# Optimization experiments

Hardware: AMD Instinct MI355X
Metric: run time of the kernel (lower is better)

## Reference

```python
import jax, jax.numpy as jnp
import numpy as np

H = 512  # hidden size
E = 512  # embedding / input size
V = 10000  # vocab size


def _lstm_cell(x, h, c, W_ih, W_hh, b_ih, b_hh):
    # torch LSTMCell gate order: i, f, g, o
    gates = x @ W_ih.T + h @ W_hh.T + b_ih + b_hh
    i, f, g, o = jnp.split(gates, 4, axis=-1)
    i = jax.nn.sigmoid(i)
    f = jax.nn.sigmoid(f)
    g = jnp.tanh(g)
    o = jax.nn.sigmoid(o)
    c_new = f * c + i * g
    h_new = o * jnp.tanh(c_new)
    return h_new, c_new


def setup_inputs() -> dict:
    key = jax.random.key(0)
    ks = jax.random.split(key, 14)
    T, B, U = 128, 32, 1024
    s = 0.05
    return {
        "inputs": jax.random.normal(ks[0], (T, B, E), jnp.float32),
        "h0": jax.random.normal(ks[1], (2, B, H), jnp.float32),
        "c0": jax.random.normal(ks[2], (2, B, H), jnp.float32),
        "listener_outputs": jax.random.normal(ks[3], (U, B, H), jnp.float32),
        "W_ih1": jax.random.normal(ks[4], (4 * H, E), jnp.float32) * s,
        "W_hh1": jax.random.normal(ks[5], (4 * H, H), jnp.float32) * s,
        "b_ih1": jax.random.normal(ks[6], (4 * H,), jnp.float32) * s,
        "b_hh1": jax.random.normal(ks[7], (4 * H,), jnp.float32) * s,
        "W_ih2": jax.random.normal(ks[8], (4 * H, H), jnp.float32) * s,
        "W_hh2": jax.random.normal(ks[9], (4 * H, H), jnp.float32) * s,
        "b_ih2": jax.random.normal(ks[10], (4 * H,), jnp.float32) * s,
        "b_hh2": jax.random.normal(ks[11], (4 * H,), jnp.float32) * s,
        "W_out": jax.random.normal(ks[12], (V, H), jnp.float32) * s,
        "b_out": jax.random.normal(ks[13], (V,), jnp.float32) * s,
    }


def reference(inputs, h0, c0, listener_outputs,
              W_ih1, W_hh1, b_ih1, b_hh1,
              W_ih2, W_hh2, b_ih2, b_hh2,
              W_out, b_out):
    # layer-1 LSTMCell + dot-product attention per timestep
    def step1(carry, x_t):
        h1, c1 = carry
        h1, c1 = _lstm_cell(x_t, h1, c1, W_ih1, W_hh1, b_ih1, b_hh1)
        # scores over listener time U: (B, U)
        scores = jnp.einsum('ubh,bh->bu', listener_outputs, h1)
        w = jax.nn.softmax(scores, axis=1)
        ctx = jnp.einsum('ubh,bu->bh', listener_outputs, w)  # (B, H)
        return (h1, c1), ctx

    (_, _), contexts = jax.lax.scan(step1, (h0[0], c0[0]), inputs)  # (T, B, H)

    # layer-2 single-layer LSTM over attention contexts
    def step2(carry, x_t):
        h2, c2 = carry
        h2, c2 = _lstm_cell(x_t, h2, c2, W_ih2, W_hh2, b_ih2, b_hh2)
        return (h2, c2), h2

    (_, _), hs = jax.lax.scan(step2, (h0[1], c0[1]), contexts)  # (T, B, H)

    logits = hs @ W_out.T + b_out  # (T, B, V)
    return jax.nn.softmax(logits, axis=2)
```

## Files before the change

kernel.cpp:

```cpp
#include <hip/hip_runtime.h>

#define T_STEPS 128
#define BATCH   32
#define HID     512
#define EMB     512
#define ULEN    1024
#define VOCAB   10000
#define G4H     2048

#define ARR_STRIDE 16
#define GO_OFF     4096
#define GO_STRIDE  64
#define BAR_WORDS  6144

static inline int cdiv(int a, int b) { return (a + b - 1) / b; }

template <bool TRANSB>
__global__ __launch_bounds__(256)
void gemm_f32(const float* __restrict__ A, long lda, long sA,
              const float* __restrict__ Bm, long ldb, long sB,
              float* __restrict__ C, long ldc, long sC,
              int M, int N, int K, const float* __restrict__ bias)
{
    __shared__ float As[16][68];
    __shared__ float Bs[16][68];
    const int bz = blockIdx.z;
    A  += (size_t)bz * sA;
    Bm += (size_t)bz * sB;
    C  += (size_t)bz * sC;
    const int m0 = blockIdx.y * 64;
    const int n0 = blockIdx.x * 64;
    const int tid = threadIdx.x;
    const int tx = tid & 15, ty = tid >> 4;
    const int lr = tid >> 2;
    const int lk = (tid & 3) * 4;

    float acc[4][4] = {{0.f}};

    for (int k0 = 0; k0 < K; k0 += 16) {
        float4 av = *(const float4*)(A + (size_t)(m0 + lr) * lda + (k0 + lk));
        As[lk + 0][lr] = av.x; As[lk + 1][lr] = av.y;
        As[lk + 2][lr] = av.z; As[lk + 3][lr] = av.w;
        if (TRANSB) {
            const int nr = n0 + lr;
            float4 bv = make_float4(0.f, 0.f, 0.f, 0.f);
            if (nr < N) bv = *(const float4*)(Bm + (size_t)nr * ldb + (k0 + lk));
            Bs[lk + 0][lr] = bv.x; Bs[lk + 1][lr] = bv.y;
            Bs[lk + 2][lr] = bv.z; Bs[lk + 3][lr] = bv.w;
        } else {
            const int kr = tid >> 4;
            const int nc = (tid & 15) * 4;
            float4 bv = make_float4(0.f, 0.f, 0.f, 0.f);
            if (n0 + nc < N) bv = *(const float4*)(Bm + (size_t)(k0 + kr) * ldb + (n0 + nc));
            *(float4*)&Bs[kr][nc] = bv;
        }
        __syncthreads();
#pragma unroll
        for (int kk = 0; kk < 16; ++kk) {
            float ar[4], br[4];
#pragma unroll
            for (int i = 0; i < 4; i++) ar[i] = As[kk][ty * 4 + i];
#pragma unroll
            for (int j = 0; j < 4; j++) br[j] = Bs[kk][tx * 4 + j];
#pragma unroll
            for (int i = 0; i < 4; i++)
#pragma unroll
                for (int j = 0; j < 4; j++)
                    acc[i][j] += ar[i] * br[j];
        }
        __syncthreads();
    }
#pragma unroll
    for (int i = 0; i < 4; i++) {
        const int row = m0 + ty * 4 + i;
#pragma unroll
        for (int j = 0; j < 4; j++) {
            const int col = n0 + tx * 4 + j;
            if (col < N) {
                float v = acc[i][j];
                if (bias) v += bias[col];
                C[(size_t)row * ldc + col] = v;
            }
        }
    }
}

__device__ inline float sigmoidf_(float x) { return 1.f / (1.f + expf(-x)); }

__global__ __launch_bounds__(256, 1)
void lstm_scan(const float* __restrict__ gp,
               const float* __restrict__ Whh,
               const float* __restrict__ h0,
               const float* __restrict__ c0,
               float* __restrict__ h_all,
               unsigned* __restrict__ bar)
{
    __shared__ float h_lds[BATCH * HID];
    __shared__ float part[256 * 36];
    unsigned* arrive = bar;
    unsigned* go     = bar + GO_OFF;

    const int tid  = threadIdx.x;
    const int bid  = blockIdx.x;
    const int hbase = bid * 2;

    const int ks = tid >> 3;
    const int nc = tid & 7;
    const int kl = ks & 7;

    const int b    = tid >> 3;
    const int nl   = tid & 7;
    const int j    = nl & 1;
    const int lane = tid & 63;
    const int sbase = lane & ~7;
    const int n = ((nl >> 1) << 9) + hbase + j;

    float4 w0, w1, w2, w3;
    {
        const int nd = ((nc >> 1) << 9) + hbase + (nc & 1);
        const float4* wsrc = (const float4*)(Whh + (size_t)nd * HID + ks * 16);
        w0 = wsrc[0]; w1 = wsrc[1]; w2 = wsrc[2]; w3 = wsrc[3];
    }

    const float* hp0 = h_lds + ((((ks * 4 + 0) ^ kl)) << 2);
    const float* hp1 = h_lds + ((((ks * 4 + 1) ^ kl)) << 2);
    const float* hp2 = h_lds + ((((ks * 4 + 2) ^ kl)) << 2);
    const float* hp3 = h_lds + ((((ks * 4 + 3) ^ kl)) << 2);

    float c_state = (nl < 2) ? c0[b * HID + hbase + j] : 0.f;

    for (int t = 0; t < T_STEPS; ++t) {
        float gval = gp[((size_t)t * BATCH + b) * G4H + n];

        const float* hsrc = (t == 0) ? h0 : (h_all + (size_t)(t - 1) * (BATCH * HID));
#pragma unroll
        for (int i = 0; i < 16; ++i) {
            const int vi = i * 256 + tid;
            float4 v = *(const float4*)(hsrc + (size_t)vi * 4);
            const int bb = vi >> 7;
            const int f  = vi & 127;
            const int p  = f ^ ((f >> 2) & 7);
            *(float4*)&h_lds[(bb << 9) + (p << 2)] = v;
        }
        __syncthreads();

        float acc[32];
#pragma unroll
        for (int b2 = 0; b2 < 32; ++b2) {
            const int o = b2 << 9;
            float4 ha = *(const float4*)(hp0 + o);
            float4 hb = *(const float4*)(hp1 + o);
            float4 hc = *(const float4*)(hp2 + o);
            float4 hd = *(const float4*)(hp3 + o);
            acc[b2] = (ha.x * w0.x + ha.y * w0.y + ha.z * w0.z + ha.w * w0.w)
                    + (hb.x * w1.x + hb.y * w1.y + hb.z * w1.z + hb.w * w1.w)
                    + (hc.x * w2.x + hc.y * w2.y + hc.z * w2.z + hc.w * w2.w)
                    + (hd.x * w3.x + hd.y * w3.y + hd.z * w3.z + hd.w * w3.w);
        }
        {
            float* pw = &part[tid * 36];
#pragma unroll
            for (int i = 0; i < 8; ++i)
                *(float4*)(pw + i * 4) =
                    make_float4(acc[4 * i], acc[4 * i + 1], acc[4 * i + 2], acc[4 * i + 3]);
        }
        __syncthreads();

        float s = gval;
        {
            const float* pr = &part[nl * 36 + b];
#pragma unroll
            for (int kr = 0; kr < 32; ++kr) s += pr[kr * 288];
        }

        float fva = __shfl(s, sbase + 2 + j);
        float gva = __shfl(s, sbase + 4 + j);
        float ova = __shfl(s, sbase + 6 + j);
        if (nl < 2) {
            float iv = sigmoidf_(s);
            float fv = sigmoidf_(fva);
            float gv = tanhf(gva);
            float ov = sigmoidf_(ova);
            c_state = fv * c_state + iv * gv;
            float hn = ov * tanhf(c_state);
            __hip_atomic_store(h_all + ((size_t)t * BATCH + b) * HID + hbase + j,
                               hn, __ATOMIC_RELAXED, __HIP_MEMORY_SCOPE_AGENT);
        }

        __syncthreads();
        const unsigned want = (unsigned)(t + 1);
        if (bid == 0) {
            if (tid == 0)
                __hip_atomic_store(&arrive[0], want, __ATOMIC_RELAXED,
                                   __HIP_MEMORY_SCOPE_AGENT);
            unsigned v;
            do {
                v = __hip_atomic_load(&arrive[tid * ARR_STRIDE], __ATOMIC_RELAXED,
                                      __HIP_MEMORY_SCOPE_AGENT);
            } while (__syncthreads_count(v >= want) < 256);
            if (tid < 32)
                __hip_atomic_store(&go[tid * GO_STRIDE], want, __ATOMIC_RELAXED,
                                   __HIP_MEMORY_SCOPE_AGENT);
        } else if (tid == 0) {
            __hip_atomic_store(&arrive[bid * ARR_STRIDE], want, __ATOMIC_RELAXED,
                               __HIP_MEMORY_SCOPE_AGENT);
            unsigned g;
            do {
                __builtin_amdgcn_s_sleep(1);
                g = __hip_atomic_load(&go[(bid & 31) * GO_STRIDE], __ATOMIC_RELAXED,
                                      __HIP_MEMORY_SCOPE_AGENT);
            } while (g < want);
        }
        __syncthreads();
    }
}

__device__ inline float warpReduceMax_(float v) {
#pragma unroll
    for (int o = 32; o > 0; o >>= 1) v = fmaxf(v, __shfl_xor(v, o));
    return v;
}
__device__ inline float warpReduceSum_(float v) {
#pragma unroll
    for (int o = 32; o > 0; o >>= 1) v += __shfl_xor(v, o);
    return v;
}
__device__ inline float blockReduceMax_(float v, float* red) {
    v = warpReduceMax_(v);
    if ((threadIdx.x & 63) == 0) red[threadIdx.x >> 6] = v;
    __syncthreads();
    float r = fmaxf(fmaxf(red[0], red[1]), fmaxf(red[2], red[3]));
    __syncthreads();
    return r;
}
__device__ inline float blockReduceSum_(float v, float* red) {
    v = warpReduceSum_(v);
    if ((threadIdx.x & 63) == 0) red[threadIdx.x >> 6] = v;
    __syncthreads();
    float r = (red[0] + red[1]) + (red[2] + red[3]);
    __syncthreads();
    return r;
}

__global__ __launch_bounds__(256)
void softmax_u(float* __restrict__ s)
{
    __shared__ float red[4];
    float4* p = (float4*)(s + (size_t)blockIdx.x * ULEN);
    float4 v = p[threadIdx.x];
    float mx = fmaxf(fmaxf(v.x, v.y), fmaxf(v.z, v.w));
    mx = blockReduceMax_(mx, red);
    v.x = expf(v.x - mx); v.y = expf(v.y - mx);
    v.z = expf(v.z - mx); v.w = expf(v.w - mx);
    float sm = blockReduceSum_(v.x + v.y + v.z + v.w, red);
    float inv = 1.f / sm;
    v.x *= inv; v.y *= inv; v.z *= inv; v.w *= inv;
    p[threadIdx.x] = v;
}

__global__ __launch_bounds__(256)
void softmax_v(float* __restrict__ out)
{
    __shared__ float buf[VOCAB];
    __shared__ float red[4];
    float* p = out + (size_t)blockIdx.x * VOCAB;
    float mx = -INFINITY;
    for (int i = threadIdx.x; i < VOCAB; i += 256) {
        float x = p[i]; buf[i] = x; mx = fmaxf(mx, x);
    }
    mx = blockReduceMax_(mx, red);
    float sm = 0.f;
    for (int i = threadIdx.x; i < VOCAB; i += 256) {
        float e = expf(buf[i] - mx); buf[i] = e; sm += e;
    }
    sm = blockReduceSum_(sm, red);
    float inv = 1.f / sm;
    for (int i = threadIdx.x; i < VOCAB; i += 256) p[i] = buf[i] * inv;
}

__global__ void prep(const float* __restrict__ bi1, const float* __restrict__ bh1,
                     const float* __restrict__ bi2, const float* __restrict__ bh2,
                     float* __restrict__ bias1, float* __restrict__ bias2,
                     unsigned* __restrict__ flags)
{
    int i = blockIdx.x * 256 + threadIdx.x;
    if (i < G4H) { bias1[i] = bi1[i] + bh1[i]; bias2[i] = bi2[i] + bh2[i]; }
    if (i < 2 * BAR_WORDS) flags[i] = 0u;
}

extern "C" void kernel_launch(void* const* d_in, const int* in_sizes, int n_in,
                              void* d_out, int out_size, void* d_ws, size_t ws_size,
                              hipStream_t stream)
{
    const float* inputs = (const float*)d_in[0];
    const float* h0     = (const float*)d_in[1];
    const float* c0     = (const float*)d_in[2];
    const float* L      = (const float*)d_in[3];
    const float* W_ih1  = (const float*)d_in[4];
    const float* W_hh1  = (const float*)d_in[5];
    const float* b_ih1  = (const float*)d_in[6];
    const float* b_hh1  = (const float*)d_in[7];
    const float* W_ih2  = (const float*)d_in[8];
    const float* W_hh2  = (const float*)d_in[9];
    const float* b_ih2  = (const float*)d_in[10];
    const float* b_hh2  = (const float*)d_in[11];
    const float* W_out  = (const float*)d_in[12];
    const float* b_out  = (const float*)d_in[13];
    float* out = (float*)d_out;

    float* ws    = (float*)d_ws;
    float* gates = ws;
    float* h1    = gates + (size_t)T_STEPS * BATCH * G4H;
    float* h2    = h1    + (size_t)T_STEPS * BATCH * HID;
    float* ctx   = h2    + (size_t)T_STEPS * BATCH * HID;
    float* bias1 = ctx   + (size_t)T_STEPS * BATCH * HID;
    float* bias2 = bias1 + G4H;
    unsigned* flags = (unsigned*)(bias2 + G4H);
    float* scores = gates;

    prep<<<48, 256, 0, stream>>>(b_ih1, b_hh1, b_ih2, b_hh2, bias1, bias2, flags);

    gemm_f32<true><<<dim3(G4H / 64, (T_STEPS * BATCH) / 64, 1), 256, 0, stream>>>(
        inputs, EMB, 0, W_ih1, EMB, 0, gates, G4H, 0,
        T_STEPS * BATCH, G4H, EMB, bias1);

    lstm_scan<<<256, 256, 0, stream>>>(gates, W_hh1, h0, c0, h1, flags);

    gemm_f32<true><<<dim3(ULEN / 64, T_STEPS / 64, BATCH), 256, 0, stream>>>(
        h1, (long)BATCH * HID, HID,
        L,  (long)BATCH * HID, HID,
        scores, (long)BATCH * ULEN, ULEN,
        T_STEPS, ULEN, HID, nullptr);

    softmax_u<<<T_STEPS * BATCH, 256, 0, stream>>>(scores);

    gemm_f32<false><<<dim3(HID / 64, T_STEPS / 64, BATCH), 256, 0, stream>>>(
        scores, (long)BATCH * ULEN, ULEN,
        L,      (long)BATCH * HID,  HID,
        ctx,    (long)BATCH * HID,  HID,
        T_STEPS, HID, ULEN, nullptr);

    gemm_f32<true><<<dim3(G4H / 64, (T_STEPS * BATCH) / 64, 1), 256, 0, stream>>>(
        ctx, HID, 0, W_ih2, HID, 0, gates, G4H, 0,
        T_STEPS * BATCH, G4H, HID, bias2);

    lstm_scan<<<256, 256, 0, stream>>>(gates, W_hh2, h0 + BATCH * HID, c0 + BATCH * HID,
                                       h2, flags + BAR_WORDS);

    gemm_f32<true><<<dim3(cdiv(VOCAB, 64), (T_STEPS * BATCH) / 64, 1), 256, 0, stream>>>(
        h2, HID, 0, W_out, HID, 0, out, VOCAB, 0,
        T_STEPS * BATCH, VOCAB, HID, b_out);

    softmax_v<<<T_STEPS * BATCH, 256, 0, stream>>>(out);
}
```

Before: 2.661 ms.

## Re-tile LSTM recurrent matvec for register reuse and prefetch next gate input

Changes the per-thread work split in the persistent LSTM scan from one gate column by 32 batch rows to 8 gate columns by 4 batch rows. Each thread now keeps 128 W_hh values in registers, so every h vector loaded from LDS is reused across 8 columns and LDS read traffic per step drops. The partial-sum layout and the reduction indexing are updated to match. The next timestep's precomputed input-gate value is also loaded ahead of the barrier to hide global latency. The cost is much higher register pressure, which could cause spills at 256 threads.

```diff
diff --git a/kernel.cpp b/kernel.cpp
--- a/kernel.cpp
+++ b/kernel.cpp
@@ -104,8 +104,8 @@
     const int bid  = blockIdx.x;
     const int hbase = bid * 2;
 
-    const int ks = tid >> 3;
-    const int nc = tid & 7;
+    const int ks = tid & 31;
+    const int bq = tid >> 5;
     const int kl = ks & 7;
 
     const int b    = tid >> 3;
@@ -115,11 +115,13 @@
     const int sbase = lane & ~7;
     const int n = ((nl >> 1) << 9) + hbase + j;
 
-    float4 w0, w1, w2, w3;
-    {
-        const int nd = ((nc >> 1) << 9) + hbase + (nc & 1);
+    float4 w[8][4];
+#pragma unroll
+    for (int col = 0; col < 8; ++col) {
+        const int nd = ((col >> 1) << 9) + hbase + (col & 1);
         const float4* wsrc = (const float4*)(Whh + (size_t)nd * HID + ks * 16);
-        w0 = wsrc[0]; w1 = wsrc[1]; w2 = wsrc[2]; w3 = wsrc[3];
+#pragma unroll
+        for (int i = 0; i < 4; ++i) w[col][i] = wsrc[i];
     }
 
     const float* hp0 = h_lds + ((((ks * 4 + 0) ^ kl)) << 2);
@@ -128,9 +130,10 @@
     const float* hp3 = h_lds + ((((ks * 4 + 3) ^ kl)) << 2);
 
     float c_state = (nl < 2) ? c0[b * HID + hbase + j] : 0.f;
+    float gnext = gp[(size_t)b * G4H + n];
 
     for (int t = 0; t < T_STEPS; ++t) {
-        float gval = gp[((size_t)t * BATCH + b) * G4H + n];
+        float gval = gnext;
 
         const float* hsrc = (t == 0) ? h0 : (h_all + (size_t)(t - 1) * (BATCH * HID));
 #pragma unroll
@@ -146,16 +149,24 @@
 
         float acc[32];
 #pragma unroll
-        for (int b2 = 0; b2 < 32; ++b2) {
-            const int o = b2 << 9;
+        for (int rr = 0; rr < 4; ++rr) {
+            const int o = (bq * 4 + rr) << 9;
             float4 ha = *(const float4*)(hp0 + o);
             float4 hb = *(const float4*)(hp1 + o);
             float4 hc = *(const float4*)(hp2 + o);
             float4 hd = *(const float4*)(hp3 + o);
-            acc[b2] = (ha.x * w0.x + ha.y * w0.y + ha.z * w0.z + ha.w * w0.w)
-                    + (hb.x * w1.x + hb.y * w1.y + hb.z * w1.z + hb.w * w1.w)
-                    + (hc.x * w2.x + hc.y * w2.y + hc.z * w2.z + hc.w * w2.w)
-                    + (hd.x * w3.x + hd.y * w3.y + hd.z * w3.z + hd.w * w3.w);
+#pragma unroll
+            for (int col = 0; col < 8; ++col) {
+                acc[rr * 8 + col] =
+                      (ha.x * w[col][0].x + ha.y * w[col][0].y
+                     + ha.z * w[col][0].z + ha.w * w[col][0].w)
+                    + (hb.x * w[col][1].x + hb.y * w[col][1].y
+                     + hb.z * w[col][1].z + hb.w * w[col][1].w)
+                    + (hc.x * w[col][2].x + hc.y * w[col][2].y
+                     + hc.z * w[col][2].z + hc.w * w[col][2].w)
+                    + (hd.x * w[col][3].x + hd.y * w[col][3].y
+                     + hd.z * w[col][3].z + hd.w * w[col][3].w);
+            }
         }
         {
             float* pw = &part[tid * 36];
@@ -168,9 +179,9 @@
 
         float s = gval;
         {
-            const float* pr = &part[nl * 36 + b];
-#pragma unroll
-            for (int kr = 0; kr < 32; ++kr) s += pr[kr * 288];
+            const float* pr = &part[(b >> 2) * (32 * 36) + (b & 3) * 8 + nl];
+#pragma unroll
+            for (int kr = 0; kr < 32; ++kr) s += pr[kr * 36];
         }
 
         float fva = __shfl(s, sbase + 2 + j);
@@ -185,6 +196,11 @@
             float hn = ov * tanhf(c_state);
             __hip_atomic_store(h_all + ((size_t)t * BATCH + b) * HID + hbase + j,
                                hn, __ATOMIC_RELAXED, __HIP_MEMORY_SCOPE_AGENT);
+        }
+
+        {
+            const int tn = (t + 1 < T_STEPS) ? (t + 1) : t;
+            gnext = gp[((size_t)tn * BATCH + b) * G4H + n];
         }
 
         __syncthreads();
```

Result: slower. 2.808 ms (+5.5%).
